# Optimization experiments

Hardware: AMD Instinct MI355X
Metric: run time of the kernel (lower is better)

## Reference

```python
import jax, jax.numpy as jnp
import numpy as np

GRID_RES = 128      # dense voxel grid standing in for octree leaves
BASIS_DIM = 9       # SH degree 2
DATA_DIM = 3 * BASIS_DIM + 1  # 27 SH color coeffs + 1 density
N_RAYS = 65536
N_STEPS = 128       # fixed ray-marching steps (replaces per-voxel traversal)
STEP_SIZE = 0.001
BG = 1.0            # background_brightness


def sh_basis9(d):
    # real SH basis, deg <= 2, svox component order/signs. d: [B,3] unit dirs
    x, y, z = d[..., 0], d[..., 1], d[..., 2]
    xx, yy, zz = x * x, y * y, z * z
    return jnp.stack([
        jnp.full_like(x, 0.28209479177387814),
        -0.4886025119029199 * y,
        0.4886025119029199 * z,
        -0.4886025119029199 * x,
        1.0925484305920792 * x * y,
        -1.0925484305920792 * y * z,
        0.31539156525252005 * (2.0 * zz - xx - yy),
        -1.0925484305920792 * x * z,
        0.5462742152960396 * (xx - yy),
    ], axis=-1)


def dda_unit(cen, invdir):
    # ray/unit-cube AABB intersection, vectorized over rays
    t1 = -cen * invdir
    t2 = t1 + invdir
    tmin = jnp.maximum(jnp.max(jnp.minimum(t1, t2), axis=-1), 0.0)
    tmax = jnp.minimum(jnp.min(jnp.maximum(t1, t2), axis=-1), 1e9)
    return tmin, tmax


def setup_inputs() -> dict:
    key = jax.random.key(0)
    k1, k2, k3, k4 = jax.random.split(key, 4)
    data = jax.random.normal(k1, (GRID_RES, GRID_RES, GRID_RES, DATA_DIM), jnp.float32) * 0.5
    origins = jax.random.uniform(k2, (N_RAYS, 3), jnp.float32, 0.1, 0.9)
    dirs = jax.random.normal(k3, (N_RAYS, 3), jnp.float32)
    viewdirs = jax.random.normal(k4, (N_RAYS, 3), jnp.float32)
    return {"data": data, "origins": origins, "dirs": dirs, "viewdirs": viewdirs}


def reference(data, origins, dirs, viewdirs):
    dirs = dirs / jnp.linalg.norm(dirs, axis=-1, keepdims=True)
    viewdirs = viewdirs / jnp.linalg.norm(viewdirs, axis=-1, keepdims=True)
    invdirs = 1.0 / (dirs + 1e-9)
    tmin, tmax = dda_unit(origins, invdirs)        # [B], [B]
    dt = jnp.maximum(tmax - tmin, 0.0) / N_STEPS   # per-ray step length
    delta_t = dt + STEP_SIZE                       # eps per step, as in svox
    sh_mult = sh_basis9(viewdirs)                  # [B, BASIS_DIM]
    B = origins.shape[0]

    def step(carry, i):
        light, out = carry                         # [B], [B,3]
        t = tmin + (i.astype(jnp.float32) + 0.5) * dt
        pos = origins + t[:, None] * dirs          # [B,3] in [0,1]
        idx = jnp.clip((pos * GRID_RES).astype(jnp.int32), 0, GRID_RES - 1)
        vals = data[idx[:, 0], idx[:, 1], idx[:, 2]]  # [B, DATA_DIM]
        sigma = jax.nn.relu(vals[:, -1])
        att = jnp.exp(-delta_t * sigma)
        weight = light * (1.0 - att)
        rgb_sh = vals[:, :-1].reshape(B, 3, BASIS_DIM)
        rgb = jax.nn.sigmoid(jnp.einsum('bk,bck->bc', sh_mult, rgb_sh))
        out = out + weight[:, None] * rgb
        return (light * att, out), None

    init = (jnp.ones((B,), jnp.float32), jnp.zeros((B, 3), jnp.float32))
    (light, out), _ = jax.lax.scan(step, init, jnp.arange(N_STEPS))
    return out + BG * light[:, None]
```

## Files before the change

### kernel.cpp

```cpp
#include <hip/hip_runtime.h>

#define GRID_RES 128
#define N_RAYS 65536
#define N_STEPS 128
#define STEP_SIZE 0.001f

__device__ __forceinline__ float sigmoidf_fast(float x) {
    return 1.0f / (1.0f + __expf(-x));
}

__device__ __forceinline__ float quad_dpp_xor1(float x) {
    return __int_as_float(__builtin_amdgcn_update_dpp(0, __float_as_int(x), 0xB1, 0xF, 0xF, true));
}
__device__ __forceinline__ float quad_dpp_xor2(float x) {
    return __int_as_float(__builtin_amdgcn_update_dpp(0, __float_as_int(x), 0x4E, 0xF, 0xF, true));
}
__device__ __forceinline__ float quad_sum(float x) {
    x += quad_dpp_xor1(x);
    x += quad_dpp_xor2(x);
    return x;
}

__global__ __launch_bounds__(256) void vr_kernel(
    const float* __restrict__ data,
    const float* __restrict__ origins,
    const float* __restrict__ dirs,
    const float* __restrict__ viewdirs,
    float* __restrict__ out)
{
    int gid = blockIdx.x * blockDim.x + threadIdx.x;
    int ray = gid >> 2;
    int l   = gid & 3;

    float ox = origins[3*ray+0], oy = origins[3*ray+1], oz = origins[3*ray+2];
    float dx = dirs[3*ray+0],    dy = dirs[3*ray+1],    dz = dirs[3*ray+2];
    float vx = viewdirs[3*ray+0], vy = viewdirs[3*ray+1], vz = viewdirs[3*ray+2];

    {
        float s = __fadd_rn(__fadd_rn(__fmul_rn(dx,dx), __fmul_rn(dy,dy)), __fmul_rn(dz,dz));
        float n = sqrtf(s);
        dx = __fdiv_rn(dx, n); dy = __fdiv_rn(dy, n); dz = __fdiv_rn(dz, n);
    }
    {
        float s = __fadd_rn(__fadd_rn(__fmul_rn(vx,vx), __fmul_rn(vy,vy)), __fmul_rn(vz,vz));
        float n = sqrtf(s);
        vx = __fdiv_rn(vx, n); vy = __fdiv_rn(vy, n); vz = __fdiv_rn(vz, n);
    }

    float invx = __fdiv_rn(1.0f, __fadd_rn(dx, 1e-9f));
    float invy = __fdiv_rn(1.0f, __fadd_rn(dy, 1e-9f));
    float invz = __fdiv_rn(1.0f, __fadd_rn(dz, 1e-9f));

    float t1x = __fmul_rn(-ox, invx), t1y = __fmul_rn(-oy, invy), t1z = __fmul_rn(-oz, invz);
    float t2x = __fadd_rn(t1x, invx), t2y = __fadd_rn(t1y, invy), t2z = __fadd_rn(t1z, invz);
    float tmin = fmaxf(fmaxf(fminf(t1x,t2x), fminf(t1y,t2y)), fminf(t1z,t2z));
    tmin = fmaxf(tmin, 0.0f);
    float tmax = fminf(fminf(fmaxf(t1x,t2x), fmaxf(t1y,t2y)), fmaxf(t1z,t2z));
    tmax = fminf(tmax, 1e9f);
    float dt = __fmul_rn(fmaxf(__fsub_rn(tmax, tmin), 0.0f), (1.0f/(float)N_STEPS));
    float delta_t = __fadd_rn(dt, STEP_SIZE);

    const float sh0 = 0.28209479177387814f;
    float sh1 = -0.4886025119029199f * vy;
    float sh2 =  0.4886025119029199f * vz;
    float sh3 = -0.4886025119029199f * vx;
    float sh4 =  1.0925484305920792f * vx * vy;
    float sh5 = -1.0925484305920792f * vy * vz;
    float sh6 =  0.31539156525252005f * (2.0f*vz*vz - vx*vx - vy*vy);
    float sh7 = -1.0925484305920792f * vx * vz;
    float sh8 =  0.5462742152960396f * (vx*vx - vy*vy);

    float wr[8], wg[8], wb[8];
    #pragma unroll
    for (int m = 0; m < 8; ++m) {
        int c  = 8*l + m;
        int cb = c % 9;
        float s = sh0;
        s = (cb==1) ? sh1 : s;
        s = (cb==2) ? sh2 : s;
        s = (cb==3) ? sh3 : s;
        s = (cb==4) ? sh4 : s;
        s = (cb==5) ? sh5 : s;
        s = (cb==6) ? sh6 : s;
        s = (cb==7) ? sh7 : s;
        s = (cb==8) ? sh8 : s;
        wr[m] = (c < 9)            ? s : 0.0f;
        wg[m] = (c >= 9 && c < 18) ? s : 0.0f;
        wb[m] = (c >= 18 && c < 27)? s : 0.0f;
    }

    unsigned offA = 8u * (unsigned)l;
    unsigned offB = (l < 3) ? (8u * (unsigned)l + 4u) : 24u;

    auto linidx = [&](int i) -> unsigned {
        float t = __fadd_rn(tmin, __fmul_rn((float)i + 0.5f, dt));
        float px = __fadd_rn(ox, __fmul_rn(t, dx));
        float py = __fadd_rn(oy, __fmul_rn(t, dy));
        float pz = __fadd_rn(oz, __fmul_rn(t, dz));
        int ix = (int)(px * (float)GRID_RES);
        int iy = (int)(py * (float)GRID_RES);
        int iz = (int)(pz * (float)GRID_RES);
        ix = min(max(ix, 0), GRID_RES-1);
        iy = min(max(iy, 0), GRID_RES-1);
        iz = min(max(iz, 0), GRID_RES-1);
        return (unsigned)(((ix << 7) | iy) << 7 | iz);
    };

    float light = 1.0f;
    float o_r = 0.0f, o_g = 0.0f, o_b = 0.0f;

    unsigned lin1;
    float s0, s1;
    float4 A0, B0;
    {
        unsigned lin0 = linidx(0);
        lin1 = linidx(1);
        s0 = data[28u * lin0 + 27u];
        s1 = data[28u * lin1 + 27u];
        const float* rec0 = (s0 > 0.0f) ? (data + 28u * lin0) : data;
        A0 = *(const float4*)(rec0 + offA);
        B0 = *(const float4*)(rec0 + offB);
    }

    for (int i = 0; i < N_STEPS; ++i) {
        unsigned lin2 = linidx(i + 2);
        float s2 = data[28u * lin2 + 27u];

        const float* rec1 = (s1 > 0.0f) ? (data + 28u * lin1) : data;
        float4 A1 = *(const float4*)(rec1 + offA);
        float4 B1 = *(const float4*)(rec1 + offB);

        float sigma = fmaxf(s0, 0.0f);
        float att = __expf(-delta_t * sigma);
        float w = light * (1.0f - att);

        float pr = wr[0]*A0.x + wr[1]*A0.y + wr[2]*A0.z + wr[3]*A0.w
                 + wr[4]*B0.x + wr[5]*B0.y + wr[6]*B0.z + wr[7]*B0.w;
        float pg = wg[0]*A0.x + wg[1]*A0.y + wg[2]*A0.z + wg[3]*A0.w
                 + wg[4]*B0.x + wg[5]*B0.y + wg[6]*B0.z + wg[7]*B0.w;
        float pb = wb[0]*A0.x + wb[1]*A0.y + wb[2]*A0.z + wb[3]*A0.w
                 + wb[4]*B0.x + wb[5]*B0.y + wb[6]*B0.z + wb[7]*B0.w;

        float r = quad_sum(pr);
        float g = quad_sum(pg);
        float b = quad_sum(pb);

        o_r = fmaf(w, sigmoidf_fast(r), o_r);
        o_g = fmaf(w, sigmoidf_fast(g), o_g);
        o_b = fmaf(w, sigmoidf_fast(b), o_b);
        light *= att;

        s0 = s1; s1 = s2;
        lin1 = lin2;
        A0 = A1; B0 = B1;
    }

    if (l == 0) {
        out[3*ray+0] = o_r + light;
        out[3*ray+1] = o_g + light;
        out[3*ray+2] = o_b + light;
    }
}

extern "C" void kernel_launch(void* const* d_in, const int* in_sizes, int n_in,
                              void* d_out, int out_size, void* d_ws, size_t ws_size,
                              hipStream_t stream) {
    const float* data     = (const float*)d_in[0];
    const float* origins  = (const float*)d_in[1];
    const float* dirs     = (const float*)d_in[2];
    const float* viewdirs = (const float*)d_in[3];
    float* out = (float*)d_out;

    dim3 block(256);
    dim3 grid((N_RAYS * 4) / 256);
    vr_kernel<<<grid, block, 0, stream>>>(data, origins, dirs, viewdirs, out);
}
```

Baseline: 122.0 us.

## Sort rays by origin cell and direction octant before marching for locality

Adds a counting-sort pass (histogram, scan, scatter) that buckets rays by a coarse origin cell and direction octant. The march kernel then reads rays through the permutation, and block indices are swizzled so each XCD gets contiguous buckets. The goal is coherent voxel gathers and better cache reuse of the 235MB grid. The cost is three extra kernel launches plus a memset and one scattered indirection per ray.

Measured after the change: 138.1 us. +13.2%, slower.

```diff
diff --git a/kernel.cpp b/kernel.cpp
--- a/kernel.cpp
+++ b/kernel.cpp
@@ -4,6 +4,7 @@
 #define N_RAYS 65536
 #define N_STEPS 128
 #define STEP_SIZE 0.001f
+#define NBUCKET 8192
 
 __device__ __forceinline__ float sigmoidf_fast(float x) {
     return 1.0f / (1.0f + __expf(-x));
@@ -19,6 +20,64 @@
     x += quad_dpp_xor1(x);
     x += quad_dpp_xor2(x);
     return x;
+}
+
+__device__ __forceinline__ unsigned ray_key(const float* __restrict__ origins,
+                                            const float* __restrict__ dirs, int r) {
+    float ox = origins[3*r+0], oy = origins[3*r+1], oz = origins[3*r+2];
+    float dx = dirs[3*r+0],    dy = dirs[3*r+1],    dz = dirs[3*r+2];
+    int qx = min(max((int)(ox * 16.0f), 0), 15);
+    int qy = min(max((int)(oy *  8.0f), 0), 7);
+    int qz = min(max((int)(oz *  8.0f), 0), 7);
+    int oct = ((dx < 0.0f) ? 4 : 0) | ((dy < 0.0f) ? 2 : 0) | ((dz < 0.0f) ? 1 : 0);
+    return (unsigned)((((((qx << 3) | qy) << 3) | qz) << 3) | oct);
+}
+
+__global__ __launch_bounds__(256) void hist_kernel(
+    const float* __restrict__ origins, const float* __restrict__ dirs,
+    unsigned* __restrict__ cnt)
+{
+    int r = blockIdx.x * blockDim.x + threadIdx.x;
+    if (r < N_RAYS) atomicAdd(&cnt[ray_key(origins, dirs, r)], 1u);
+}
+
+__global__ __launch_bounds__(1024) void scan_kernel(
+    const unsigned* __restrict__ cnt, unsigned* __restrict__ offs)
+{
+    __shared__ unsigned s[1024];
+    int tid = threadIdx.x;
+    unsigned local[NBUCKET / 1024];
+    unsigned sum = 0;
+    #pragma unroll
+    for (int m = 0; m < NBUCKET / 1024; ++m) {
+        local[m] = cnt[tid * (NBUCKET / 1024) + m];
+        sum += local[m];
+    }
+    s[tid] = sum;
+    __syncthreads();
+    for (int off = 1; off < 1024; off <<= 1) {
+        unsigned v = (tid >= off) ? s[tid - off] : 0u;
+        __syncthreads();
+        s[tid] += v;
+        __syncthreads();
+    }
+    unsigned run = (tid > 0) ? s[tid - 1] : 0u;
+    #pragma unroll
+    for (int m = 0; m < NBUCKET / 1024; ++m) {
+        offs[tid * (NBUCKET / 1024) + m] = run;
+        run += local[m];
+    }
+}
+
+__global__ __launch_bounds__(256) void scatter_kernel(
+    const float* __restrict__ origins, const float* __restrict__ dirs,
+    unsigned* __restrict__ offs, unsigned* __restrict__ perm)
+{
+    int r = blockIdx.x * blockDim.x + threadIdx.x;
+    if (r < N_RAYS) {
+        unsigned pos = atomicAdd(&offs[ray_key(origins, dirs, r)], 1u);
+        perm[pos] = (unsigned)r;
+    }
 }
 
 __global__ __launch_bounds__(256) void vr_kernel(
@@ -26,11 +85,13 @@
     const float* __restrict__ origins,
     const float* __restrict__ dirs,
     const float* __restrict__ viewdirs,
+    const unsigned* __restrict__ perm,
     float* __restrict__ out)
 {
-    int gid = blockIdx.x * blockDim.x + threadIdx.x;
-    int ray = gid >> 2;
-    int l   = gid & 3;
+    unsigned wg = (blockIdx.x & 7u) * (gridDim.x >> 3) + (blockIdx.x >> 3);
+    unsigned q  = wg * 64u + ((unsigned)threadIdx.x >> 2);
+    int ray = (int)perm[q];
+    int l   = threadIdx.x & 3;
 
     float ox = origins[3*ray+0], oy = origins[3*ray+1], oz = origins[3*ray+2];
     float dx = dirs[3*ray+0],    dy = dirs[3*ray+1],    dz = dirs[3*ray+2];
@@ -70,7 +131,7 @@
     float sh7 = -1.0925484305920792f * vx * vz;
     float sh8 =  0.5462742152960396f * (vx*vx - vy*vy);
 
-    float wr[8], wg[8], wb[8];
+    float wr[8], wg_[8], wb[8];
     #pragma unroll
     for (int m = 0; m < 8; ++m) {
         int c  = 8*l + m;
@@ -84,9 +145,9 @@
         s = (cb==6) ? sh6 : s;
         s = (cb==7) ? sh7 : s;
         s = (cb==8) ? sh8 : s;
-        wr[m] = (c < 9)            ? s : 0.0f;
-        wg[m] = (c >= 9 && c < 18) ? s : 0.0f;
-        wb[m] = (c >= 18 && c < 27)? s : 0.0f;
+        wr[m]  = (c < 9)            ? s : 0.0f;
+        wg_[m] = (c >= 9 && c < 18) ? s : 0.0f;
+        wb[m]  = (c >= 18 && c < 27)? s : 0.0f;
     }
 
     unsigned offA = 8u * (unsigned)l;
@@ -136,8 +197,8 @@
 
         float pr = wr[0]*A0.x + wr[1]*A0.y + wr[2]*A0.z + wr[3]*A0.w
                  + wr[4]*B0.x + wr[5]*B0.y + wr[6]*B0.z + wr[7]*B0.w;
-        float pg = wg[0]*A0.x + wg[1]*A0.y + wg[2]*A0.z + wg[3]*A0.w
-                 + wg[4]*B0.x + wg[5]*B0.y + wg[6]*B0.z + wg[7]*B0.w;
+        float pg = wg_[0]*A0.x + wg_[1]*A0.y + wg_[2]*A0.z + wg_[3]*A0.w
+                 + wg_[4]*B0.x + wg_[5]*B0.y + wg_[6]*B0.z + wg_[7]*B0.w;
         float pb = wb[0]*A0.x + wb[1]*A0.y + wb[2]*A0.z + wb[3]*A0.w
                  + wb[4]*B0.x + wb[5]*B0.y + wb[6]*B0.z + wb[7]*B0.w;
 
@@ -171,7 +232,16 @@
     const float* viewdirs = (const float*)d_in[3];
     float* out = (float*)d_out;
 
+    unsigned* cnt  = (unsigned*)d_ws;
+    unsigned* offs = cnt + NBUCKET;
+    unsigned* perm = offs + NBUCKET;
+
+    hipMemsetAsync(cnt, 0, NBUCKET * sizeof(unsigned), stream);
+    hist_kernel<<<N_RAYS / 256, 256, 0, stream>>>(origins, dirs, cnt);
+    scan_kernel<<<1, 1024, 0, stream>>>(cnt, offs);
+    scatter_kernel<<<N_RAYS / 256, 256, 0, stream>>>(origins, dirs, offs, perm);
+
     dim3 block(256);
     dim3 grid((N_RAYS * 4) / 256);
-    vr_kernel<<<grid, block, 0, stream>>>(data, origins, dirs, viewdirs, out);
-}
+    vr_kernel<<<grid, block, 0, stream>>>(data, origins, dirs, viewdirs, perm, out);
+}
```

## Split each ray across eight lanes with one float4 load per lane

Applied to the files above, without the earlier changes.

Each ray is now handled by eight lanes instead of four. Each lane loads a single float4 of the voxel record rather than two, and the reduction adds a ds_swizzle xor-4 step to sum across the eight lanes. Launch bounds request higher occupancy and the grid is doubled. The aim is more memory-level parallelism and fewer per-thread registers, at the cost of duplicated per-ray setup and index math across lanes and an extra cross-lane step on the LDS path.

Result: slower. 177.2 us (+45.3%).

```diff
diff --git a/kernel.cpp b/kernel.cpp
--- a/kernel.cpp
+++ b/kernel.cpp
@@ -9,19 +9,23 @@
     return 1.0f / (1.0f + __expf(-x));
 }
 
-__device__ __forceinline__ float quad_dpp_xor1(float x) {
+__device__ __forceinline__ float oct_dpp_xor1(float x) {
     return __int_as_float(__builtin_amdgcn_update_dpp(0, __float_as_int(x), 0xB1, 0xF, 0xF, true));
 }
-__device__ __forceinline__ float quad_dpp_xor2(float x) {
+__device__ __forceinline__ float oct_dpp_xor2(float x) {
     return __int_as_float(__builtin_amdgcn_update_dpp(0, __float_as_int(x), 0x4E, 0xF, 0xF, true));
 }
-__device__ __forceinline__ float quad_sum(float x) {
-    x += quad_dpp_xor1(x);
-    x += quad_dpp_xor2(x);
+__device__ __forceinline__ float oct_swz_xor4(float x) {
+    return __int_as_float(__builtin_amdgcn_ds_swizzle(__float_as_int(x), 0x101F));
+}
+__device__ __forceinline__ float oct_sum(float x) {
+    x += oct_dpp_xor1(x);
+    x += oct_dpp_xor2(x);
+    x += oct_swz_xor4(x);
     return x;
 }
 
-__global__ __launch_bounds__(256) void vr_kernel(
+__global__ __launch_bounds__(256, 8) void vr_kernel(
     const float* __restrict__ data,
     const float* __restrict__ origins,
     const float* __restrict__ dirs,
@@ -29,8 +33,8 @@
     float* __restrict__ out)
 {
     int gid = blockIdx.x * blockDim.x + threadIdx.x;
-    int ray = gid >> 2;
-    int l   = gid & 3;
+    int ray = gid >> 3;
+    int l   = gid & 7;
 
     float ox = origins[3*ray+0], oy = origins[3*ray+1], oz = origins[3*ray+2];
     float dx = dirs[3*ray+0],    dy = dirs[3*ray+1],    dz = dirs[3*ray+2];
@@ -70,10 +74,10 @@
     float sh7 = -1.0925484305920792f * vx * vz;
     float sh8 =  0.5462742152960396f * (vx*vx - vy*vy);
 
-    float wr[8], wg[8], wb[8];
+    float wr[4], wg[4], wb[4];
     #pragma unroll
-    for (int m = 0; m < 8; ++m) {
-        int c  = 8*l + m;
+    for (int m = 0; m < 4; ++m) {
+        int c  = (l < 7) ? (4*l + m) : 27;
         int cb = c % 9;
         float s = sh0;
         s = (cb==1) ? sh1 : s;
@@ -89,8 +93,7 @@
         wb[m] = (c >= 18 && c < 27)? s : 0.0f;
     }
 
-    unsigned offA = 8u * (unsigned)l;
-    unsigned offB = (l < 3) ? (8u * (unsigned)l + 4u) : 24u;
+    unsigned offC = (l < 7) ? (4u * (unsigned)l) : 24u;
 
     auto linidx = [&](int i) -> unsigned {
         float t = __fadd_rn(tmin, __fmul_rn((float)i + 0.5f, dt));
@@ -111,15 +114,14 @@
 
     unsigned lin1;
     float s0, s1;
-    float4 A0, B0;
+    float4 C0;
     {
         unsigned lin0 = linidx(0);
         lin1 = linidx(1);
         s0 = data[28u * lin0 + 27u];
         s1 = data[28u * lin1 + 27u];
         const float* rec0 = (s0 > 0.0f) ? (data + 28u * lin0) : data;
-        A0 = *(const float4*)(rec0 + offA);
-        B0 = *(const float4*)(rec0 + offB);
+        C0 = *(const float4*)(rec0 + offC);
     }
 
     for (int i = 0; i < N_STEPS; ++i) {
@@ -127,23 +129,19 @@
         float s2 = data[28u * lin2 + 27u];
 
         const float* rec1 = (s1 > 0.0f) ? (data + 28u * lin1) : data;
-        float4 A1 = *(const float4*)(rec1 + offA);
-        float4 B1 = *(const float4*)(rec1 + offB);
+        float4 C1 = *(const float4*)(rec1 + offC);
 
         float sigma = fmaxf(s0, 0.0f);
         float att = __expf(-delta_t * sigma);
         float w = light * (1.0f - att);
 
-        float pr = wr[0]*A0.x + wr[1]*A0.y + wr[2]*A0.z + wr[3]*A0.w
-                 + wr[4]*B0.x + wr[5]*B0.y + wr[6]*B0.z + wr[7]*B0.w;
-        float pg = wg[0]*A0.x + wg[1]*A0.y + wg[2]*A0.z + wg[3]*A0.w
-                 + wg[4]*B0.x + wg[5]*B0.y + wg[6]*B0.z + wg[7]*B0.w;
-        float pb = wb[0]*A0.x + wb[1]*A0.y + wb[2]*A0.z + wb[3]*A0.w
-                 + wb[4]*B0.x + wb[5]*B0.y + wb[6]*B0.z + wb[7]*B0.w;
+        float pr = wr[0]*C0.x + wr[1]*C0.y + wr[2]*C0.z + wr[3]*C0.w;
+        float pg = wg[0]*C0.x + wg[1]*C0.y + wg[2]*C0.z + wg[3]*C0.w;
+        float pb = wb[0]*C0.x + wb[1]*C0.y + wb[2]*C0.z + wb[3]*C0.w;
 
-        float r = quad_sum(pr);
-        float g = quad_sum(pg);
-        float b = quad_sum(pb);
+        float r = oct_sum(pr);
+        float g = oct_sum(pg);
+        float b = oct_sum(pb);
 
         o_r = fmaf(w, sigmoidf_fast(r), o_r);
         o_g = fmaf(w, sigmoidf_fast(g), o_g);
@@ -152,7 +150,7 @@
 
         s0 = s1; s1 = s2;
         lin1 = lin2;
-        A0 = A1; B0 = B1;
+        C0 = C1;
     }
 
     if (l == 0) {
@@ -172,6 +170,6 @@
     float* out = (float*)d_out;
 
     dim3 block(256);
-    dim3 grid((N_RAYS * 4) / 256);
+    dim3 grid((N_RAYS * 8) / 256);
     vr_kernel<<<grid, block, 0, stream>>>(data, origins, dirs, viewdirs, out);
 }
```

## Precompute per-voxel density sign bitmask and read sigma from the record

Applied to the files above, without the earlier changes.

Adds a pre-pass kernel that scans every voxel's density and writes a 1-bit-per-voxel occupancy mask into workspace. The marching kernel then tests this small, cache-friendly mask instead of issuing a separate density gather for each sample. Sigma itself is taken from the already-loaded record via a quad DPP broadcast. Sigmoid now uses a hardware reciprocal, and the launch bounds add an occupancy hint. The trade-off is that the pre-pass reads the density of all voxels on every call, which strides through most of the large grid and may cost more than the per-sample loads it removes.

Result: slower. 131.3 us (+7.6%).

```diff
diff --git a/kernel.cpp b/kernel.cpp
--- a/kernel.cpp
+++ b/kernel.cpp
@@ -4,9 +4,13 @@
 #define N_RAYS 65536
 #define N_STEPS 128
 #define STEP_SIZE 0.001f
-
+#define NVOX (GRID_RES * GRID_RES * GRID_RES)
+
+__device__ __forceinline__ float rcp_fast(float x) {
+    return __builtin_amdgcn_rcpf(x);
+}
 __device__ __forceinline__ float sigmoidf_fast(float x) {
-    return 1.0f / (1.0f + __expf(-x));
+    return rcp_fast(1.0f + __expf(-x));
 }
 
 __device__ __forceinline__ float quad_dpp_xor1(float x) {
@@ -14,6 +18,9 @@
 }
 __device__ __forceinline__ float quad_dpp_xor2(float x) {
     return __int_as_float(__builtin_amdgcn_update_dpp(0, __float_as_int(x), 0x4E, 0xF, 0xF, true));
+}
+__device__ __forceinline__ float quad_bcast3(float x) {
+    return __int_as_float(__builtin_amdgcn_update_dpp(0, __float_as_int(x), 0xFF, 0xF, 0xF, true));
 }
 __device__ __forceinline__ float quad_sum(float x) {
     x += quad_dpp_xor1(x);
@@ -21,11 +28,21 @@
     return x;
 }
 
-__global__ __launch_bounds__(256) void vr_kernel(
+__global__ __launch_bounds__(256) void sigma_mask_kernel(
+    const float* __restrict__ data, unsigned long long* __restrict__ mask)
+{
+    int v = blockIdx.x * blockDim.x + threadIdx.x;
+    float s = data[28u * (unsigned)v + 27u];
+    unsigned long long b = __ballot(s > 0.0f);
+    if ((threadIdx.x & 63) == 0) mask[(unsigned)v >> 6] = b;
+}
+
+__global__ __launch_bounds__(256, 4) void vr_kernel(
     const float* __restrict__ data,
     const float* __restrict__ origins,
     const float* __restrict__ dirs,
     const float* __restrict__ viewdirs,
+    const unsigned long long* __restrict__ mask,
     float* __restrict__ out)
 {
     int gid = blockIdx.x * blockDim.x + threadIdx.x;
@@ -70,7 +87,7 @@
     float sh7 = -1.0925484305920792f * vx * vz;
     float sh8 =  0.5462742152960396f * (vx*vx - vy*vy);
 
-    float wr[8], wg[8], wb[8];
+    float wr[8], wg_[8], wb[8];
     #pragma unroll
     for (int m = 0; m < 8; ++m) {
         int c  = 8*l + m;
@@ -84,9 +101,9 @@
         s = (cb==6) ? sh6 : s;
         s = (cb==7) ? sh7 : s;
         s = (cb==8) ? sh8 : s;
-        wr[m] = (c < 9)            ? s : 0.0f;
-        wg[m] = (c >= 9 && c < 18) ? s : 0.0f;
-        wb[m] = (c >= 18 && c < 27)? s : 0.0f;
+        wr[m]  = (c < 9)            ? s : 0.0f;
+        wg_[m] = (c >= 9 && c < 18) ? s : 0.0f;
+        wb[m]  = (c >= 18 && c < 27)? s : 0.0f;
     }
 
     unsigned offA = 8u * (unsigned)l;
@@ -106,38 +123,43 @@
         return (unsigned)(((ix << 7) | iy) << 7 | iz);
     };
 
+    auto maskbit = [&](unsigned lin) -> bool {
+        unsigned long long w = mask[lin >> 6];
+        return (w >> (lin & 63u)) & 1ull;
+    };
+
     float light = 1.0f;
     float o_r = 0.0f, o_g = 0.0f, o_b = 0.0f;
 
     unsigned lin1;
-    float s0, s1;
+    bool b0, b1;
     float4 A0, B0;
     {
         unsigned lin0 = linidx(0);
         lin1 = linidx(1);
-        s0 = data[28u * lin0 + 27u];
-        s1 = data[28u * lin1 + 27u];
-        const float* rec0 = (s0 > 0.0f) ? (data + 28u * lin0) : data;
+        b0 = maskbit(lin0);
+        b1 = maskbit(lin1);
+        const float* rec0 = b0 ? (data + 28u * lin0) : data;
         A0 = *(const float4*)(rec0 + offA);
         B0 = *(const float4*)(rec0 + offB);
     }
 
     for (int i = 0; i < N_STEPS; ++i) {
         unsigned lin2 = linidx(i + 2);
-        float s2 = data[28u * lin2 + 27u];
-
-        const float* rec1 = (s1 > 0.0f) ? (data + 28u * lin1) : data;
+        bool b2 = maskbit(lin2);
+
+        const float* rec1 = b1 ? (data + 28u * lin1) : data;
         float4 A1 = *(const float4*)(rec1 + offA);
         float4 B1 = *(const float4*)(rec1 + offB);
 
-        float sigma = fmaxf(s0, 0.0f);
+        float sigma = b0 ? quad_bcast3(A0.w) : 0.0f;
         float att = __expf(-delta_t * sigma);
         float w = light * (1.0f - att);
 
         float pr = wr[0]*A0.x + wr[1]*A0.y + wr[2]*A0.z + wr[3]*A0.w
                  + wr[4]*B0.x + wr[5]*B0.y + wr[6]*B0.z + wr[7]*B0.w;
-        float pg = wg[0]*A0.x + wg[1]*A0.y + wg[2]*A0.z + wg[3]*A0.w
-                 + wg[4]*B0.x + wg[5]*B0.y + wg[6]*B0.z + wg[7]*B0.w;
+        float pg = wg_[0]*A0.x + wg_[1]*A0.y + wg_[2]*A0.z + wg_[3]*A0.w
+                 + wg_[4]*B0.x + wg_[5]*B0.y + wg_[6]*B0.z + wg_[7]*B0.w;
         float pb = wb[0]*A0.x + wb[1]*A0.y + wb[2]*A0.z + wb[3]*A0.w
                  + wb[4]*B0.x + wb[5]*B0.y + wb[6]*B0.z + wb[7]*B0.w;
 
@@ -150,7 +172,7 @@
         o_b = fmaf(w, sigmoidf_fast(b), o_b);
         light *= att;
 
-        s0 = s1; s1 = s2;
+        b0 = b1; b1 = b2;
         lin1 = lin2;
         A0 = A1; B0 = B1;
     }
@@ -171,7 +193,8 @@
     const float* viewdirs = (const float*)d_in[3];
     float* out = (float*)d_out;
 
-    dim3 block(256);
-    dim3 grid((N_RAYS * 4) / 256);
-    vr_kernel<<<grid, block, 0, stream>>>(data, origins, dirs, viewdirs, out);
-}
+    unsigned long long* mask = (unsigned long long*)d_ws;
+
+    sigma_mask_kernel<<<NVOX / 256, 256, 0, stream>>>(data, mask);
+    vr_kernel<<<(N_RAYS * 4) / 256, 256, 0, stream>>>(data, origins, dirs, viewdirs, mask, out);
+}
```
